# Optimization experiments

Measured on AMD Instinct MI355X. Metric: run time of the kernel, lower is better.

## Reference

```python
import jax, jax.numpy as jnp
import numpy as np

CUTOFF = 5.0
EPS = 1e-8
N_BASIS = 20
N_LAYERS = 3
F = 128
B, A, N = 4, 256, 64
ZMAX = 100


def _linear(x, W, b=None):
    y = jnp.einsum('...i,oi->...o', x, W)
    return y + b if b is not None else y


def _mlp(x, W1, b1, W2, b2):
    return _linear(jax.nn.silu(_linear(x, W1, b1)), W2, b2)


def _poly_cutoff(d):
    # PolynomialCutoff with p = 6
    p = 6.0
    x = d / CUTOFF
    f = (1.0 - ((p + 1.0) * (p + 2.0) / 2.0) * x**6
         + p * (p + 2.0) * x**7
         - (p * (p + 1.0) / 2.0) * x**8)
    return f * (x < 1.0).astype(d.dtype)


def _rbf(d):
    # RadialBesselLayer: sin(n*pi*d/cutoff) / d, n = 1..N_BASIS
    n = jnp.arange(1, N_BASIS + 1, dtype=d.dtype)
    return jnp.sin(n * jnp.pi * d[..., None] / CUTOFF) / (d[..., None] + EPS)


def _gather(feats, neighbors):
    # feats [B,A,...], neighbors [B,A,N] -> [B,A,N,...]
    return jax.vmap(lambda f, idx: f[idx])(feats, neighbors)


def setup_inputs() -> dict:
    key = jax.random.key(0)
    ks = iter(jax.random.split(key, 64))
    s = 0.08  # weight scale
    inp = {
        'atomic_numbers': jax.random.randint(next(ks), (B, A), 0, ZMAX),
        'positions': jax.random.normal(next(ks), (B, A, 3), jnp.float32),
        'neighbors': jax.random.randint(next(ks), (B, A, N), 0, A),
        'neighbor_mask': jnp.ones((B, A, N), jnp.float32),
        'distances': jax.random.uniform(next(ks), (B, A, N), jnp.float32, 0.1, 4.9),
        'distance_vectors': jax.random.normal(next(ks), (B, A, N, 3), jnp.float32),
        'emb': jax.random.normal(next(ks), (ZMAX, F), jnp.float32) * 0.5,
        'me_W': jax.random.normal(next(ks), (N_LAYERS, F, N_BASIS), jnp.float32) * s,
        'me_b': jnp.zeros((N_LAYERS, F), jnp.float32),
        'mn_W1': jax.random.normal(next(ks), (N_LAYERS, F, F), jnp.float32) * s,
        'mn_b1': jnp.zeros((N_LAYERS, F), jnp.float32),
        'mn_W2': jax.random.normal(next(ks), (N_LAYERS, F, F), jnp.float32) * s,
        'mn_b2': jnp.zeros((N_LAYERS, F), jnp.float32),
        'eqc_W': jax.random.normal(next(ks), (N_LAYERS, 1, F), jnp.float32) * s,
        'eqf_W1': jax.random.normal(next(ks), (N_LAYERS, F, F), jnp.float32) * s,
        'eqf_b1': jnp.zeros((N_LAYERS, F), jnp.float32),
        'eqf_W2': jax.random.normal(next(ks), (N_LAYERS, F, F), jnp.float32) * s,
        'eqf_b2': jnp.zeros((N_LAYERS, F), jnp.float32),
        'esu_W1': jax.random.normal(next(ks), (N_LAYERS, F, F), jnp.float32) * s,
        'esu_b1': jnp.zeros((N_LAYERS, F), jnp.float32),
        'esu_W2': jax.random.normal(next(ks), (N_LAYERS, F, F), jnp.float32) * s,
        'esu_b2': jnp.zeros((N_LAYERS, F), jnp.float32),
        'eme_W1': jax.random.normal(next(ks), (N_LAYERS, F, F), jnp.float32) * s,
        'eme_W2': jax.random.normal(next(ks), (N_LAYERS, F, F), jnp.float32) * s,
        'isu_W1': jax.random.normal(next(ks), (N_LAYERS, F, F), jnp.float32) * s,
        'isu_b1': jnp.zeros((N_LAYERS, F), jnp.float32),
        'isu_W2': jax.random.normal(next(ks), (N_LAYERS, F, F), jnp.float32) * s,
        'isu_b2': jnp.zeros((N_LAYERS, F), jnp.float32),
    }
    return inp


def _forward(atomic_numbers, neighbors, neighbor_mask, distances, distance_vectors,
             emb, me_W, me_b, mn_W1, mn_b1, mn_W2, mn_b2, eqc_W,
             eqf_W1, eqf_b1, eqf_W2, eqf_b2, esu_W1, esu_b1, esu_W2, esu_b2,
             eme_W1, eme_W2, isu_W1, isu_b1, isu_W2, isu_b2):
    # ---- EmbeddingNet ----
    inv_node = emb[atomic_numbers]                      # [B,A,F]
    b, a, f = inv_node.shape
    eq_F = jnp.zeros((b, a, 3), inv_node.dtype)         # [B,A,3]
    eq_f = jnp.zeros((b, a, 3, f), inv_node.dtype)      # [B,A,3,F]
    eq_dr = jnp.zeros((b, a, 3, f), inv_node.dtype)     # [B,A,3,F]
    unit = distance_vectors / (distances[..., None] + EPS)  # [B,A,N,3]
    inv_edge = _rbf(distances)                          # [B,A,N,n_basis]
    cutoff = _poly_cutoff(distances)[..., None]         # [B,A,N,1]
    mask = neighbor_mask[..., None]                     # [B,A,N,1]
    mask2 = neighbor_mask[..., None, None]              # [B,A,N,1,1]

    # ---- InteractionNet x N_LAYERS ----
    for l in range(N_LAYERS):
        msg_edge = _linear(inv_edge, me_W[l], me_b[l]) * cutoff           # [B,A,N,F]
        msg_node = _mlp(inv_node, mn_W1[l], mn_b1[l], mn_W2[l], mn_b2[l])  # [B,A,F]
        msg_node_i = msg_node[:, :, None, :]                               # [B,A,1,F]
        msg_node_f = _gather(msg_node, neighbors)                          # [B,A,N,F]
        inv_msg = msg_edge * msg_node_i * msg_node_f                       # [B,A,N,F]
        # double_update_node = False -> no early invariant update
        eq_msg_F = _linear(inv_msg, eqc_W[l]) * unit                       # [B,A,N,3]
        eq_upd_F = (eq_msg_F * mask).sum(axis=2)                           # [B,A,3]
        eq_F = eq_F + eq_upd_F
        eq_msg_feat = _mlp(inv_msg, eqf_W1[l], eqf_b1[l], eqf_W2[l], eqf_b2[l])
        eq_msg_f = eq_msg_feat[..., None, :] * eq_msg_F[..., None]         # [B,A,N,3,F]
        eq_upd_f = (eq_msg_f * mask2).sum(axis=2)                          # [B,A,3,F]
        eq_f = eq_f + eq_upd_f
        dr_edge = _linear(jax.nn.silu(_linear(inv_msg, eme_W1[l])), eme_W2[l])[..., None, :]  # [B,A,N,1,F]
        dr_node_f = _gather(eq_dr, neighbors)                              # [B,A,N,3,F]
        eq_upd_dr = (dr_edge * dr_node_f * mask2).sum(axis=2)              # [B,A,3,F]
        eq_dr = eq_dr + eq_upd_dr
        eq_dr = eq_dr + _mlp(inv_node, esu_W1[l], esu_b1[l], esu_W2[l], esu_b2[l])[:, :, None, :] * eq_upd_f
        inv_upd = -_mlp(inv_node, isu_W1[l], isu_b1[l], isu_W2[l], isu_b2[l]) * jnp.sum(eq_f * eq_dr, axis=-2)
        inv_node = inv_node + inv_upd
    return inv_node, eq_F, eq_f, eq_dr


def reference(atomic_numbers, positions, neighbors, neighbor_mask, distances, distance_vectors,
              emb, me_W, me_b, mn_W1, mn_b1, mn_W2, mn_b2, eqc_W,
              eqf_W1, eqf_b1, eqf_W2, eqf_b2, esu_W1, esu_b1, esu_W2, esu_b2,
              eme_W1, eme_W2, isu_W1, isu_b1, isu_W2, isu_b2):
    # positions unused (requires_dr = False in EmbeddingNet)
    return _forward(atomic_numbers, neighbors, neighbor_mask, distances, distance_vectors,
                    emb, me_W, me_b, mn_W1, mn_b1, mn_W2, mn_b2, eqc_W,
                    eqf_W1, eqf_b1, eqf_W2, eqf_b2, esu_W1, esu_b1, esu_W2, esu_b2,
                    eme_W1, eme_W2, isu_W1, isu_b1, isu_W2, isu_b2)
```

## Files before the change

kernel.cpp:

```cpp
#include <hip/hip_runtime.h>
#include <cstdint>
#include <cstddef>

#define BB   4
#define AA   256
#define NNB  64
#define FF   128
#define NBAS 20
#define NLAY 3
#define BA   (BB*AA)
#define EDG  (BA*NNB)

typedef __attribute__((ext_vector_type(8))) short bf16x8;
typedef __attribute__((ext_vector_type(4))) float f32x4;

__device__ __forceinline__ float silu_f(float x){ return x / (1.0f + __expf(-x)); }

__device__ __forceinline__ unsigned short f2bf(float x){
  unsigned int u = __float_as_uint(x);
  u += 0x7FFFu + ((u >> 16) & 1u);
  return (unsigned short)(u >> 16);
}
__device__ __forceinline__ unsigned int pk2(float a, float b){
  unsigned int r;
  asm("v_cvt_pk_bf16_f32 %0, %1, %2" : "=v"(r) : "v"(a), "v"(b));
  return r;
}

__global__ void k_cvtw(const float* __restrict__ a, const float* __restrict__ b,
                       const float* __restrict__ c, const float* __restrict__ d,
                       const float* __restrict__ me,
                       const float* __restrict__ mnW1, const float* __restrict__ mnW2,
                       const float* __restrict__ esW1, const float* __restrict__ esW2,
                       const float* __restrict__ isW1, const float* __restrict__ isW2,
                       unsigned short* __restrict__ out){
  int id = blockIdx.x*256 + threadIdx.x;
  if (id < 196608){
    int reg = id / 49152, off = id - reg*49152;
    const float* src = (reg==0)?a:(reg==1)?b:(reg==2)?c:d;
    out[id] = f2bf(src[off]);
  } else if (id < 208896){
    int p = id - 196608;
    int l = p >> 12;
    int rem = p & 4095;
    int row = rem >> 5, k = rem & 31;
    float v = (k < NBAS) ? me[((size_t)l*FF + row)*NBAS + k] : 0.0f;
    out[id] = f2bf(v);
  } else if (id < 503808){
    int p = id - 208896;
    int mat = p / 49152, rem = p - mat*49152;
    const float* src = (mat==0)?mnW1:(mat==1)?mnW2:(mat==2)?esW1:(mat==3)?esW2:(mat==4)?isW1:isW2;
    out[id] = f2bf(src[rem]);
  }
}

__global__ __launch_bounds__(256) void k_node_mfma(
    const float* __restrict__ X, const int* __restrict__ z,
    const float* __restrict__ emb, float* __restrict__ inv_node,
    const unsigned short* W1a, const float* b1a, const unsigned short* W2a, const float* b2a, float* Ya,
    const unsigned short* W1b, const float* b1b, const unsigned short* W2b, const float* b2b, float* Yb,
    const unsigned short* W1c, const float* b1c, const unsigned short* W2c, const float* b2c, float* Yc,
    int do_emb){
  const unsigned short *W1,*W2; const float *b1,*b2; float* Y;
  if (blockIdx.y==0){ W1=W1a;b1=b1a;W2=W2a;b2=b2a;Y=Ya; }
  else if (blockIdx.y==1){ W1=W1b;b1=b1b;W2=W2b;b2=b2b;Y=Yb; }
  else { W1=W1c;b1=b1c;W2=W2c;b2=b2c;Y=Yc; }
  __shared__ unsigned short Ws[128*136];
  __shared__ unsigned short Xs[64*136];
  const int t = threadIdx.x, w = t>>6, l = t&63;
  const int g = l&15, kg = (l>>4)<<3, r0 = (l>>4)<<2;
  const int gr0 = blockIdx.x*64;
  const int le = w*16 + g;

  {
    int row = t>>2, c0 = (t&3)*32;
    const float* src = do_emb ? (emb + (size_t)z[gr0+row]*FF + c0)
                              : (X   + (size_t)(gr0+row)*FF + c0);
    #pragma unroll
    for (int j=0;j<8;++j){
      float4 v = *(const float4*)(src + j*4);
      if (do_emb && blockIdx.y==0)
        *(float4*)(inv_node + (size_t)(gr0+row)*FF + c0 + j*4) = v;
      uint2 u; u.x = pk2(v.x,v.y); u.y = pk2(v.z,v.w);
      *(uint2*)(&Xs[row*136 + c0 + j*4]) = u;
    }
  }
  #pragma unroll
  for (int c=t; c<2048; c+=256){
    int row = c >> 4, ko = (c & 15) << 3;
    *(int4*)(&Ws[row*136 + ko]) = *(const int4*)(W1 + row*FF + ko);
  }
  __syncthreads();
  bf16x8 xf[4];
  #pragma unroll
  for (int ks=0;ks<4;++ks) xf[ks] = *(const bf16x8*)(&Xs[le*136 + ks*32 + kg]);
  __syncthreads();
  f32x4 acc[8];
  #pragma unroll
  for (int nt=0;nt<8;++nt) acc[nt] = f32x4{0.f,0.f,0.f,0.f};
  #pragma unroll
  for (int nt=0;nt<8;++nt)
    #pragma unroll
    for (int ks=0;ks<4;++ks){
      bf16x8 wfr = *(const bf16x8*)(&Ws[(nt*16+g)*136 + ks*32 + kg]);
      acc[nt] = __builtin_amdgcn_mfma_f32_16x16x32_bf16(wfr, xf[ks], acc[nt], 0,0,0);
    }
  #pragma unroll
  for (int nt=0;nt<8;++nt){
    int o0 = nt*16 + r0;
    float4 bb = *(const float4*)(b1 + o0);
    uint2 u;
    u.x = pk2(silu_f(acc[nt][0]+bb.x), silu_f(acc[nt][1]+bb.y));
    u.y = pk2(silu_f(acc[nt][2]+bb.z), silu_f(acc[nt][3]+bb.w));
    *(uint2*)(&Xs[le*136 + o0]) = u;
  }
  __syncthreads();
  #pragma unroll
  for (int c=t; c<2048; c+=256){
    int row = c >> 4, ko = (c & 15) << 3;
    *(int4*)(&Ws[row*136 + ko]) = *(const int4*)(W2 + row*FF + ko);
  }
  __syncthreads();
  bf16x8 hf[4];
  #pragma unroll
  for (int ks=0;ks<4;++ks) hf[ks] = *(const bf16x8*)(&Xs[le*136 + ks*32 + kg]);
  #pragma unroll
  for (int nt=0;nt<8;++nt) acc[nt] = f32x4{0.f,0.f,0.f,0.f};
  #pragma unroll
  for (int nt=0;nt<8;++nt)
    #pragma unroll
    for (int ks=0;ks<4;++ks){
      bf16x8 wfr = *(const bf16x8*)(&Ws[(nt*16+g)*136 + ks*32 + kg]);
      acc[nt] = __builtin_amdgcn_mfma_f32_16x16x32_bf16(wfr, hf[ks], acc[nt], 0,0,0);
    }
  #pragma unroll
  for (int nt=0;nt<8;++nt){
    int o0 = nt*16 + r0;
    float4 bb = *(const float4*)(b2 + o0);
    float4 o;
    o.x = acc[nt][0]+bb.x; o.y = acc[nt][1]+bb.y;
    o.z = acc[nt][2]+bb.z; o.w = acc[nt][3]+bb.w;
    *(float4*)(Y + (size_t)(gr0 + le)*FF + o0) = o;
  }
}

__global__ __launch_bounds__(256) void k_layer(
    const float* __restrict__ dist, const float* __restrict__ dvec,
    const float* __restrict__ maskp, const int* __restrict__ nbrs,
    const float* __restrict__ msg_node,
    const unsigned short* __restrict__ meWb, const float* __restrict__ meb,
    const float* __restrict__ eqcW,
    const unsigned short* __restrict__ W1eq, const float* __restrict__ b1eq,
    const unsigned short* __restrict__ W1me,
    const unsigned short* __restrict__ W2eq, const float* __restrict__ b2eq,
    const unsigned short* __restrict__ W2me,
    const float* __restrict__ eqdrT_prev, float* __restrict__ eqdrT_next,
    const float* __restrict__ esu, const float* __restrict__ isu,
    float* __restrict__ eqF, float* __restrict__ eqf_out,
    float* __restrict__ eqdr, float* __restrict__ inv_node, int first){
  __shared__ unsigned short Ws[128*136];
  __shared__ unsigned short Hs[128*136];
  __shared__ float scal[128][4];
  __shared__ int   nbq[128];
  __shared__ float red[4][384];
  __shared__ float eqFred[4][2][3];
  const int t = threadIdx.x, w = t>>6, l = t&63;
  const int bid = blockIdx.x, a0 = bid*2;
  const int g = l&15, kg = (l>>4)<<3, r0 = (l>>4)<<2;
  const float c5 = 0.6283185307179586f;

  #pragma unroll
  for (int c=t; c<2048; c+=256){
    int row = c >> 4, ko = (c & 15) << 3;
    *(int4*)(&Hs[row*136 + ko]) = *(const int4*)(W1eq + row*FF + ko);
  }
  if (t < 128){
    int e2 = a0*NNB + t;
    int atomt = a0 + (t>>6);
    nbq[t] = (atomt/AA)*AA + nbrs[e2];
  }

  #pragma unroll
  for (int p=0;p<2;++p){
    const int atom = a0 + p;
    const int eg = atom*NNB + w*16 + g;
    const float d = dist[eg];
    const float dinv = 1.0f/(d + 1e-8f);
    const float xx = d*0.2f;
    float x2=xx*xx, x4=x2*x2, x6=x4*x2, x7=x6*xx, x8=x7*xx;
    float ct = 1.0f - 28.0f*x6 + 48.0f*x7 - 21.0f*x8;
    ct = (xx < 1.0f) ? ct : 0.0f;
    bf16x8 rfr;
    #pragma unroll
    for (int i=0;i<8;++i){
      int k = kg + i;
      float v = (k < NBAS) ? __sinf((float)(k+1)*c5*d)*dinv : 0.0f;
      rfr[i] = (short)f2bf(v);
    }
    f32x4 acc[8];
    #pragma unroll
    for (int nt=0;nt<8;++nt){
      bf16x8 wfr = *(const bf16x8*)(meWb + (nt*16 + g)*32 + kg);
      acc[nt] = __builtin_amdgcn_mfma_f32_16x16x32_bf16(wfr, rfr, f32x4{0.f,0.f,0.f,0.f}, 0,0,0);
    }
    const int bbase = (atom/AA)*AA;
    const int nbv = bbase + nbrs[eg];
    float pv = 0.f;
    #pragma unroll
    for (int nt=0;nt<8;++nt){
      int o0 = nt*16 + r0;
      float4 mb = *(const float4*)(meb + o0);
      float4 mi = *(const float4*)(msg_node + (size_t)atom*FF + o0);
      float4 mf = *(const float4*)(msg_node + (size_t)nbv*FF + o0);
      float4 ec = *(const float4*)(eqcW + o0);
      float v0 = (acc[nt][0]+mb.x)*ct*mi.x*mf.x;
      float v1 = (acc[nt][1]+mb.y)*ct*mi.y*mf.y;
      float v2 = (acc[nt][2]+mb.z)*ct*mi.z*mf.z;
      float v3 = (acc[nt][3]+mb.w)*ct*mi.w*mf.w;
      pv = fmaf(v0,ec.x, fmaf(v1,ec.y, fmaf(v2,ec.z, fmaf(v3,ec.w, pv))));
      uint2 u; u.x = pk2(v0,v1); u.y = pk2(v2,v3);
      *(uint2*)(&Ws[(p*64 + w*16 + g)*136 + o0]) = u;
    }
    pv += __shfl_xor(pv,16); pv += __shfl_xor(pv,32);
    float cf0=0.f, cf1=0.f, cf2=0.f;
    if (l < 16){
      float m  = maskp[eg];
      float s0 = pv*dvec[(size_t)eg*3+0]*dinv;
      float s1 = pv*dvec[(size_t)eg*3+1]*dinv;
      float s2 = pv*dvec[(size_t)eg*3+2]*dinv;
      int lr = p*64 + w*16 + g;
      scal[lr][0]=s0; scal[lr][1]=s1; scal[lr][2]=s2; scal[lr][3]=m;
      cf0 = s0*m; cf1 = s1*m; cf2 = s2*m;
    }
    #pragma unroll
    for (int s2=1; s2<16; s2<<=1){
      cf0 += __shfl_xor(cf0,s2); cf1 += __shfl_xor(cf1,s2); cf2 += __shfl_xor(cf2,s2);
    }
    if (l == 0){ eqFred[w][p][0]=cf0; eqFred[w][p][1]=cf1; eqFred[w][p][2]=cf2; }
  }
  __syncthreads();

  bf16x8 xf[2][4];
  #pragma unroll
  for (int ms=0;ms<2;++ms)
    #pragma unroll
    for (int ks=0;ks<4;++ks)
      xf[ms][ks] = *(const bf16x8*)(&Ws[(w*32 + ms*16 + g)*136 + ks*32 + kg]);
  if (t < 6){
    int p = t/3, c = t - p*3;
    float s = eqFred[0][p][c]+eqFred[1][p][c]+eqFred[2][p][c]+eqFred[3][p][c];
    eqF[(a0+p)*3 + c] = first ? s : (eqF[(a0+p)*3 + c] + s);
  }
  __syncthreads();

  f32x4 acc2[2][8];
  #pragma unroll
  for (int ms=0;ms<2;++ms)
    #pragma unroll
    for (int nt=0;nt<8;++nt) acc2[ms][nt] = f32x4{0.f,0.f,0.f,0.f};
  #pragma unroll
  for (int nt=0;nt<8;++nt)
    #pragma unroll
    for (int ks=0;ks<4;++ks){
      bf16x8 wfr = *(const bf16x8*)(&Hs[(nt*16+g)*136 + ks*32 + kg]);
      #pragma unroll
      for (int ms=0;ms<2;++ms)
        acc2[ms][nt] = __builtin_amdgcn_mfma_f32_16x16x32_bf16(wfr, xf[ms][ks], acc2[ms][nt], 0,0,0);
    }
  #pragma unroll
  for (int ms=0;ms<2;++ms)
    #pragma unroll
    for (int nt=0;nt<8;++nt){
      int o0 = nt*16 + r0;
      float4 bb = *(const float4*)(b1eq + o0);
      uint2 u;
      u.x = pk2(silu_f(acc2[ms][nt][0]+bb.x), silu_f(acc2[ms][nt][1]+bb.y));
      u.y = pk2(silu_f(acc2[ms][nt][2]+bb.z), silu_f(acc2[ms][nt][3]+bb.w));
      *(uint2*)(&Ws[(w*32 + ms*16 + g)*136 + o0]) = u;
    }
  __syncthreads();

  #pragma unroll
  for (int c=t; c<2048; c+=256){
    int row = c >> 4, ko = (c & 15) << 3;
    *(int4*)(&Hs[row*136 + ko]) = *(const int4*)(W2eq + row*FF + ko);
  }
  __syncthreads();
  {
    bf16x8 hfr[2][4];
    #pragma unroll
    for (int ms=0;ms<2;++ms)
      #pragma unroll
      for (int ks=0;ks<4;++ks)
        hfr[ms][ks] = *(const bf16x8*)(&Ws[(w*32 + ms*16 + g)*136 + ks*32 + kg]);
    #pragma unroll
    for (int ms=0;ms<2;++ms)
      #pragma unroll
      for (int nt=0;nt<8;++nt) acc2[ms][nt] = f32x4{0.f,0.f,0.f,0.f};
    #pragma unroll
    for (int nt=0;nt<8;++nt)
      #pragma unroll
      for (int ks=0;ks<4;++ks){
        bf16x8 wfr = *(const bf16x8*)(&Hs[(nt*16+g)*136 + ks*32 + kg]);
        #pragma unroll
        for (int ms=0;ms<2;++ms)
          acc2[ms][nt] = __builtin_amdgcn_mfma_f32_16x16x32_bf16(hfr[ms][ks], wfr, acc2[ms][nt], 0,0,0);
      }
    #pragma unroll
    for (int nt=0;nt<8;++nt){
      int col = nt*16 + g;
      float bb = b2eq[col];
      float q0=0.f,q1=0.f,q2=0.f;
      #pragma unroll
      for (int ms=0;ms<2;++ms)
        #pragma unroll
        for (int r=0;r<4;++r){
          int row = w*32 + ms*16 + r0 + r;
          float ym = (acc2[ms][nt][r] + bb) * scal[row][3];
          q0 = fmaf(ym, scal[row][0], q0);
          q1 = fmaf(ym, scal[row][1], q1);
          q2 = fmaf(ym, scal[row][2], q2);
        }
      q0 += __shfl_xor(q0,16); q0 += __shfl_xor(q0,32);
      q1 += __shfl_xor(q1,16); q1 += __shfl_xor(q1,32);
      q2 += __shfl_xor(q2,16); q2 += __shfl_xor(q2,32);
      if (l < 16){
        red[w][0*128+col] = q0; red[w][1*128+col] = q1; red[w][2*128+col] = q2;
      }
    }
  }
  __syncthreads();

  float ef_reg[3], s1_reg[3];
  {
    int k = 0;
    for (int i=t; i<768; i+=256, ++k){
      int p = (i >= 384) ? 1 : 0;
      int j = i - p*384;
      float s1 = red[2*p][j] + red[2*p+1][j];
      size_t idx = (size_t)(a0+p)*384 + j;
      float ef = first ? s1 : (eqf_out[idx] + s1);
      eqf_out[idx] = ef;
      ef_reg[k] = ef; s1_reg[k] = s1;
    }
  }

  if (!first){
    #pragma unroll
    for (int c=t; c<2048; c+=256){
      int row = c >> 4, ko = (c & 15) << 3;
      *(int4*)(&Ws[row*136 + ko]) = *(const int4*)(W1me + row*FF + ko);
    }
    __syncthreads();
    #pragma unroll
    for (int ms=0;ms<2;++ms)
      #pragma unroll
      for (int nt=0;nt<8;++nt) acc2[ms][nt] = f32x4{0.f,0.f,0.f,0.f};
    #pragma unroll
    for (int nt=0;nt<8;++nt)
      #pragma unroll
      for (int ks=0;ks<4;++ks){
        bf16x8 wfr = *(const bf16x8*)(&Ws[(nt*16+g)*136 + ks*32 + kg]);
        #pragma unroll
        for (int ms=0;ms<2;++ms)
          acc2[ms][nt] = __builtin_amdgcn_mfma_f32_16x16x32_bf16(wfr, xf[ms][ks], acc2[ms][nt], 0,0,0);
      }
    #pragma unroll
    for (int ms=0;ms<2;++ms)
      #pragma unroll
      for (int nt=0;nt<8;++nt){
        int o0 = nt*16 + r0;
        uint2 u;
        u.x = pk2(silu_f(acc2[ms][nt][0]), silu_f(acc2[ms][nt][1]));
        u.y = pk2(silu_f(acc2[ms][nt][2]), silu_f(acc2[ms][nt][3]));
        *(uint2*)(&Hs[(w*32 + ms*16 + g)*136 + o0]) = u;
      }
    __syncthreads();
    #pragma unroll
    for (int c=t; c<2048; c+=256){
      int row = c >> 4, ko = (c & 15) << 3;
      *(int4*)(&Ws[row*136 + ko]) = *(const int4*)(W2me + row*FF + ko);
    }
    __syncthreads();
    bf16x8 hfr[2][4];
    #pragma unroll
    for (int ms=0;ms<2;++ms)
      #pragma unroll
      for (int ks=0;ks<4;++ks)
        hfr[ms][ks] = *(const bf16x8*)(&Hs[(w*32 + ms*16 + g)*136 + ks*32 + kg]);
    #pragma unroll
    for (int ms=0;ms<2;++ms)
      #pragma unroll
      for (int nt=0;nt<8;++nt) acc2[ms][nt] = f32x4{0.f,0.f,0.f,0.f};
    #pragma unroll
    for (int nt=0;nt<8;++nt)
      #pragma unroll
      for (int ks=0;ks<4;++ks){
        bf16x8 wfr = *(const bf16x8*)(&Ws[(nt*16+g)*136 + ks*32 + kg]);
        #pragma unroll
        for (int ms=0;ms<2;++ms)
          acc2[ms][nt] = __builtin_amdgcn_mfma_f32_16x16x32_bf16(hfr[ms][ks], wfr, acc2[ms][nt], 0,0,0);
      }
    #pragma unroll
    for (int nt=0;nt<8;++nt){
      int col = nt*16 + g;
      float q0=0.f,q1=0.f,q2=0.f;
      #pragma unroll
      for (int ms=0;ms<2;++ms)
        #pragma unroll
        for (int r=0;r<4;++r){
          int row = w*32 + ms*16 + r0 + r;
          float ym = acc2[ms][nt][r] * scal[row][3];
          float4 gv = *(const float4*)(eqdrT_prev + ((size_t)nbq[row]*FF + col)*4);
          q0 = fmaf(ym, gv.x, q0);
          q1 = fmaf(ym, gv.y, q1);
          q2 = fmaf(ym, gv.z, q2);
        }
      q0 += __shfl_xor(q0,16); q0 += __shfl_xor(q0,32);
      q1 += __shfl_xor(q1,16); q1 += __shfl_xor(q1,32);
      q2 += __shfl_xor(q2,16); q2 += __shfl_xor(q2,32);
      if (l < 16){
        red[w][0*128+col] = q0; red[w][1*128+col] = q1; red[w][2*128+col] = q2;
      }
    }
    __syncthreads();
  }

  {
    int k = 0;
    for (int i=t; i<768; i+=256, ++k){
      int p = (i >= 384) ? 1 : 0;
      int j = i - p*384;
      int o = j & 127;
      int c = j >> 7;
      float s2 = first ? 0.0f : (red[2*p][j] + red[2*p+1][j]);
      size_t idx = (size_t)(a0+p)*384 + j;
      float es = esu[(size_t)(a0+p)*FF + o];
      float v = (first ? 0.0f : eqdr[idx]) + s2 + es*s1_reg[k];
      eqdr[idx] = v;
      eqdrT_next[((size_t)(a0+p)*FF + o)*4 + c] = v;
      red[2*p][j] = ef_reg[k] * v;
    }
  }
  __syncthreads();
  {
    int p = t >> 7, o = t & 127;
    float sum3 = red[2*p][o] + red[2*p][128+o] + red[2*p][256+o];
    size_t idx = (size_t)(a0+p)*FF + o;
    inv_node[idx] = fmaf(-isu[idx], sum3, inv_node[idx]);
  }
}

extern "C" void kernel_launch(void* const* d_in, const int* in_sizes, int n_in,
                              void* d_out, int out_size, void* d_ws, size_t ws_size,
                              hipStream_t stream){
  const int*   z     = (const int*)  d_in[0];
  const int*   nbrs  = (const int*)  d_in[2];
  const float* maskp = (const float*)d_in[3];
  const float* dist  = (const float*)d_in[4];
  const float* dvec  = (const float*)d_in[5];
  const float* emb   = (const float*)d_in[6];
  const float* me_W  = (const float*)d_in[7];
  const float* me_b  = (const float*)d_in[8];
  const float* mn_W1 = (const float*)d_in[9];
  const float* mn_b1 = (const float*)d_in[10];
  const float* mn_W2 = (const float*)d_in[11];
  const float* mn_b2 = (const float*)d_in[12];
  const float* eqc_W = (const float*)d_in[13];
  const float* eqf_W1= (const float*)d_in[14];
  const float* eqf_b1= (const float*)d_in[15];
  const float* eqf_W2= (const float*)d_in[16];
  const float* eqf_b2= (const float*)d_in[17];
  const float* esu_W1= (const float*)d_in[18];
  const float* esu_b1= (const float*)d_in[19];
  const float* esu_W2= (const float*)d_in[20];
  const float* esu_b2= (const float*)d_in[21];
  const float* eme_W1= (const float*)d_in[22];
  const float* eme_W2= (const float*)d_in[23];
  const float* isu_W1= (const float*)d_in[24];
  const float* isu_b1= (const float*)d_in[25];
  const float* isu_W2= (const float*)d_in[26];
  const float* isu_b2= (const float*)d_in[27];

  float* out      = (float*)d_out;
  float* inv_node = out;
  float* eqF      = out + 131072;
  float* eqf      = out + 134144;
  float* eqdr     = out + 527360;

  float* w        = (float*)d_ws;
  float* msg_node = w;
  float* esu_o    = w + 131072;
  float* isu_o    = w + 262144;
  float* eqdrT_A  = w + 393216;
  float* eqdrT_B  = w + 917504;
  unsigned short* wbf = (unsigned short*)(w + 1441792);

  k_cvtw<<<1968, 256, 0, stream>>>(eqf_W1, eqf_W2, eme_W1, eme_W2, me_W,
      mn_W1, mn_W2, esu_W1, esu_W2, isu_W1, isu_W2, wbf);

  const unsigned short* mnW1b0  = wbf + 208896;
  const unsigned short* mnW2b0  = wbf + 258048;
  const unsigned short* esW1b0  = wbf + 307200;
  const unsigned short* esW2b0  = wbf + 356352;
  const unsigned short* isW1b0  = wbf + 405504;
  const unsigned short* isW2b0  = wbf + 454656;

  k_node_mfma<<<dim3(BA/64, 3), 256, 0, stream>>>(nullptr, z, emb, inv_node,
      mnW1b0, mn_b1,  mnW2b0, mn_b2,  msg_node,
      esW1b0, esu_b1, esW2b0, esu_b2, esu_o,
      isW1b0, isu_b1, isW2b0, isu_b2, isu_o, 1);

  for (int l=0; l<NLAY; ++l){
    size_t oB = (size_t)l*FF;
    const unsigned short* eqfW1b = wbf + 0*49152 + l*16384;
    const unsigned short* eqfW2b = wbf + 1*49152 + l*16384;
    const unsigned short* emeW1b = wbf + 2*49152 + l*16384;
    const unsigned short* emeW2b = wbf + 3*49152 + l*16384;
    const unsigned short* meWb   = wbf + 196608  + l*4096;
    float* dT_prev = (l & 1) ? eqdrT_B : eqdrT_A;
    float* dT_next = (l & 1) ? eqdrT_A : eqdrT_B;
    int first = (l==0);

    k_layer<<<BA/2, 256, 0, stream>>>(dist, dvec, maskp, nbrs, msg_node,
        meWb, me_b+oB, eqc_W+oB,
        eqfW1b, eqf_b1+oB, emeW1b,
        eqfW2b, eqf_b2+oB, emeW2b,
        dT_prev, dT_next, esu_o, isu_o,
        eqF, eqf, eqdr, inv_node, first);
    if (l < NLAY-1){
      size_t oBn = (size_t)(l+1)*FF;
      k_node_mfma<<<dim3(BA/64, 3), 256, 0, stream>>>(inv_node, nullptr, nullptr, nullptr,
          mnW1b0 + (l+1)*16384, mn_b1+oBn,  mnW2b0 + (l+1)*16384, mn_b2+oBn,  msg_node,
          esW1b0 + (l+1)*16384, esu_b1+oBn, esW2b0 + (l+1)*16384, esu_b2+oBn, esu_o,
          isW1b0 + (l+1)*16384, isu_b1+oBn, isW2b0 + (l+1)*16384, isu_b2+oBn, isu_o, 0);
    }
  }
}
```

Before: 139.5 us.

## Stage layer weights via async global_load_lds with XOR-swizzled shared layout

Result: faster. 134.5 us (median of 2 runs) (-3.6%).

```diff
diff --git a/kernel.cpp b/kernel.cpp
--- a/kernel.cpp
+++ b/kernel.cpp
@@ -25,6 +25,10 @@
   unsigned int r;
   asm("v_cvt_pk_bf16_f32 %0, %1, %2" : "=v"(r) : "v"(a), "v"(b));
   return r;
+}
+
+__device__ __forceinline__ int swzi(int row, int us){
+  return (row << 7) + (us ^ ((row & 7) << 3));
 }
 
 __global__ void k_cvtw(const float* __restrict__ a, const float* __restrict__ b,
@@ -38,7 +42,9 @@
   if (id < 196608){
     int reg = id / 49152, off = id - reg*49152;
     const float* src = (reg==0)?a:(reg==1)?b:(reg==2)?c:d;
-    out[id] = f2bf(src[off]);
+    int lay = off >> 14, us = off & 16383;
+    int row = us >> 7, col = us & 127;
+    out[id] = f2bf(src[(lay<<14) + (row<<7) + (col ^ ((row&7)<<3))]);
   } else if (id < 208896){
     int p = id - 196608;
     int l = p >> 12;
@@ -144,6 +150,18 @@
   }
 }
 
+__device__ __forceinline__ void stage_dma(const unsigned short* Gsw,
+                                          unsigned short* buf, int w, int l){
+  const char* g = (const char*)Gsw;
+  char* bp = (char*)buf;
+  #pragma unroll
+  for (int i=0;i<8;++i){
+    __builtin_amdgcn_global_load_lds(
+        (const void*)(g + w*8192 + i*1024 + l*16),
+        (void*)(bp + w*8192 + i*1024), 16, 0, 0);
+  }
+}
+
 __global__ __launch_bounds__(256) void k_layer(
     const float* __restrict__ dist, const float* __restrict__ dvec,
     const float* __restrict__ maskp, const int* __restrict__ nbrs,
@@ -158,8 +176,8 @@
     const float* __restrict__ esu, const float* __restrict__ isu,
     float* __restrict__ eqF, float* __restrict__ eqf_out,
     float* __restrict__ eqdr, float* __restrict__ inv_node, int first){
-  __shared__ unsigned short Ws[128*136];
-  __shared__ unsigned short Hs[128*136];
+  __shared__ unsigned short Ws[128*128];
+  __shared__ unsigned short Hs[128*128];
   __shared__ float scal[128][4];
   __shared__ int   nbq[128];
   __shared__ float red[4][384];
@@ -169,11 +187,7 @@
   const int g = l&15, kg = (l>>4)<<3, r0 = (l>>4)<<2;
   const float c5 = 0.6283185307179586f;
 
-  #pragma unroll
-  for (int c=t; c<2048; c+=256){
-    int row = c >> 4, ko = (c & 15) << 3;
-    *(int4*)(&Hs[row*136 + ko]) = *(const int4*)(W1eq + row*FF + ko);
-  }
+  stage_dma(W1eq, Hs, w, l);
   if (t < 128){
     int e2 = a0*NNB + t;
     int atomt = a0 + (t>>6);
@@ -219,7 +233,7 @@
       float v3 = (acc[nt][3]+mb.w)*ct*mi.w*mf.w;
       pv = fmaf(v0,ec.x, fmaf(v1,ec.y, fmaf(v2,ec.z, fmaf(v3,ec.w, pv))));
       uint2 u; u.x = pk2(v0,v1); u.y = pk2(v2,v3);
-      *(uint2*)(&Ws[(p*64 + w*16 + g)*136 + o0]) = u;
+      *(uint2*)(&Ws[swzi(p*64 + w*16 + g, o0)]) = u;
     }
     pv += __shfl_xor(pv,16); pv += __shfl_xor(pv,32);
     float cf0=0.f, cf1=0.f, cf2=0.f;
@@ -245,7 +259,7 @@
   for (int ms=0;ms<2;++ms)
     #pragma unroll
     for (int ks=0;ks<4;++ks)
-      xf[ms][ks] = *(const bf16x8*)(&Ws[(w*32 + ms*16 + g)*136 + ks*32 + kg]);
+      xf[ms][ks] = *(const bf16x8*)(&Ws[swzi(w*32 + ms*16 + g, ks*32 + kg)]);
   if (t < 6){
     int p = t/3, c = t - p*3;
     float s = eqFred[0][p][c]+eqFred[1][p][c]+eqFred[2][p][c]+eqFred[3][p][c];
@@ -262,11 +276,13 @@
   for (int nt=0;nt<8;++nt)
     #pragma unroll
     for (int ks=0;ks<4;++ks){
-      bf16x8 wfr = *(const bf16x8*)(&Hs[(nt*16+g)*136 + ks*32 + kg]);
+      bf16x8 wfr = *(const bf16x8*)(&Hs[swzi(nt*16+g, ks*32+kg)]);
       #pragma unroll
       for (int ms=0;ms<2;++ms)
         acc2[ms][nt] = __builtin_amdgcn_mfma_f32_16x16x32_bf16(wfr, xf[ms][ks], acc2[ms][nt], 0,0,0);
     }
+  __syncthreads();
+  stage_dma(W2eq, Hs, w, l);
   #pragma unroll
   for (int ms=0;ms<2;++ms)
     #pragma unroll
@@ -276,23 +292,17 @@
       uint2 u;
       u.x = pk2(silu_f(acc2[ms][nt][0]+bb.x), silu_f(acc2[ms][nt][1]+bb.y));
       u.y = pk2(silu_f(acc2[ms][nt][2]+bb.z), silu_f(acc2[ms][nt][3]+bb.w));
-      *(uint2*)(&Ws[(w*32 + ms*16 + g)*136 + o0]) = u;
-    }
-  __syncthreads();
-
-  #pragma unroll
-  for (int c=t; c<2048; c+=256){
-    int row = c >> 4, ko = (c & 15) << 3;
-    *(int4*)(&Hs[row*136 + ko]) = *(const int4*)(W2eq + row*FF + ko);
-  }
-  __syncthreads();
+      *(uint2*)(&Ws[swzi(w*32 + ms*16 + g, o0)]) = u;
+    }
+  __syncthreads();
+
   {
     bf16x8 hfr[2][4];
     #pragma unroll
     for (int ms=0;ms<2;++ms)
       #pragma unroll
       for (int ks=0;ks<4;++ks)
-        hfr[ms][ks] = *(const bf16x8*)(&Ws[(w*32 + ms*16 + g)*136 + ks*32 + kg]);
+        hfr[ms][ks] = *(const bf16x8*)(&Ws[swzi(w*32 + ms*16 + g, ks*32 + kg)]);
     #pragma unroll
     for (int ms=0;ms<2;++ms)
       #pragma unroll
@@ -301,7 +311,7 @@
     for (int nt=0;nt<8;++nt)
       #pragma unroll
       for (int ks=0;ks<4;++ks){
-        bf16x8 wfr = *(const bf16x8*)(&Hs[(nt*16+g)*136 + ks*32 + kg]);
+        bf16x8 wfr = *(const bf16x8*)(&Hs[swzi(nt*16+g, ks*32+kg)]);
         #pragma unroll
         for (int ms=0;ms<2;++ms)
           acc2[ms][nt] = __builtin_amdgcn_mfma_f32_16x16x32_bf16(hfr[ms][ks], wfr, acc2[ms][nt], 0,0,0);
@@ -331,6 +341,8 @@
   }
   __syncthreads();
 
+  if (!first) stage_dma(W1me, Ws, w, l);
+
   float ef_reg[3], s1_reg[3];
   {
     int k = 0;
@@ -344,15 +356,10 @@
       ef_reg[k] = ef; s1_reg[k] = s1;
     }
   }
+  __syncthreads();
 
   if (!first){
     #pragma unroll
-    for (int c=t; c<2048; c+=256){
-      int row = c >> 4, ko = (c & 15) << 3;
-      *(int4*)(&Ws[row*136 + ko]) = *(const int4*)(W1me + row*FF + ko);
-    }
-    __syncthreads();
-    #pragma unroll
     for (int ms=0;ms<2;++ms)
       #pragma unroll
       for (int nt=0;nt<8;++nt) acc2[ms][nt] = f32x4{0.f,0.f,0.f,0.f};
@@ -360,11 +367,13 @@
     for (int nt=0;nt<8;++nt)
       #pragma unroll
       for (int ks=0;ks<4;++ks){
-        bf16x8 wfr = *(const bf16x8*)(&Ws[(nt*16+g)*136 + ks*32 + kg]);
+        bf16x8 wfr = *(const bf16x8*)(&Ws[swzi(nt*16+g, ks*32+kg)]);
         #pragma unroll
         for (int ms=0;ms<2;++ms)
           acc2[ms][nt] = __builtin_amdgcn_mfma_f32_16x16x32_bf16(wfr, xf[ms][ks], acc2[ms][nt], 0,0,0);
       }
+    __syncthreads();
+    stage_dma(W2me, Ws, w, l);
     #pragma unroll
     for (int ms=0;ms<2;++ms)
       #pragma unroll
@@ -373,21 +382,15 @@
         uint2 u;
         u.x = pk2(silu_f(acc2[ms][nt][0]), silu_f(acc2[ms][nt][1]));
         u.y = pk2(silu_f(acc2[ms][nt][2]), silu_f(acc2[ms][nt][3]));
-        *(uint2*)(&Hs[(w*32 + ms*16 + g)*136 + o0]) = u;
+        *(uint2*)(&Hs[swzi(w*32 + ms*16 + g, o0)]) = u;
       }
     __syncthreads();
-    #pragma unroll
-    for (int c=t; c<2048; c+=256){
-      int row = c >> 4, ko = (c & 15) << 3;
-      *(int4*)(&Ws[row*136 + ko]) = *(const int4*)(W2me + row*FF + ko);
-    }
-    __syncthreads();
     bf16x8 hfr[2][4];
     #pragma unroll
     for (int ms=0;ms<2;++ms)
       #pragma unroll
       for (int ks=0;ks<4;++ks)
-        hfr[ms][ks] = *(const bf16x8*)(&Hs[(w*32 + ms*16 + g)*136 + ks*32 + kg]);
+        hfr[ms][ks] = *(const bf16x8*)(&Hs[swzi(w*32 + ms*16 + g, ks*32 + kg)]);
     #pragma unroll
     for (int ms=0;ms<2;++ms)
       #pragma unroll
@@ -396,7 +399,7 @@
     for (int nt=0;nt<8;++nt)
       #pragma unroll
       for (int ks=0;ks<4;++ks){
-        bf16x8 wfr = *(const bf16x8*)(&Ws[(nt*16+g)*136 + ks*32 + kg]);
+        bf16x8 wfr = *(const bf16x8*)(&Ws[swzi(nt*16+g, ks*32+kg)]);
         #pragma unroll
         for (int ms=0;ms<2;++ms)
           acc2[ms][nt] = __builtin_amdgcn_mfma_f32_16x16x32_bf16(hfr[ms][ks], wfr, acc2[ms][nt], 0,0,0);
```
